# Performance work log

Measured on AMD Instinct MI355X. Metric: run time of the kernel, lower is better.

The kernel has to match this reference:

```python
import jax, jax.numpy as jnp
import numpy as np
import math

S, D = 8192, 128

def setup_inputs() -> dict:
    key = jax.random.key(0)
    kq, kk, kv = jax.random.split(key, 3)
    return {
        "q": jax.random.normal(kq, (S, D), dtype=jnp.float32),
        "k": jax.random.normal(kk, (S, D), dtype=jnp.float32),
        "v": jax.random.normal(kv, (S, D), dtype=jnp.float32),
    }

def reference(q, k, v):
    # scores: [S, S]; scale by sqrt(d) as in the torch module
    scale = 1.0 / math.sqrt(q.shape[1])
    scores = (q @ k.T) * scale
    attn = jax.nn.softmax(scores, axis=-1)
    return attn @ v
```

## Files before the change

### kernel.cpp

```cpp
#include <hip/hip_runtime.h>
#include <hip/hip_bf16.h>

#define SEQ 8192
#define HD 128
#define BM 256
#define BN 64
#define NQT (SEQ / BM)
#define THREADS 1024

typedef __bf16 bf16_t;
typedef __bf16 bf16x2 __attribute__((ext_vector_type(2)));
typedef __bf16 bf16x8 __attribute__((ext_vector_type(8)));
typedef float f32x4 __attribute__((ext_vector_type(4)));
typedef float f32x16 __attribute__((ext_vector_type(16)));
typedef unsigned int u32x4 __attribute__((ext_vector_type(4)));

#if __has_builtin(__builtin_amdgcn_exp2f)
__device__ inline float exp2_fast(float x) { return __builtin_amdgcn_exp2f(x); }
#else
__device__ inline float exp2_fast(float x) { return exp2f(x); }
#endif

__device__ inline void permswap32(unsigned int& a, unsigned int& b) {
#if __has_builtin(__builtin_amdgcn_permlane32_swap)
  auto r = __builtin_amdgcn_permlane32_swap(a, b, false, false);
  a = (unsigned int)r[0];
  b = (unsigned int)r[1];
#else
  asm volatile("v_permlane32_swap_b32 %0, %1" : "+v"(a), "+v"(b));
#endif
}

__device__ inline void load_lds16(const void* g, void* l) {
  __builtin_amdgcn_global_load_lds(
      (const __attribute__((address_space(1))) void*)g,
      (__attribute__((address_space(3))) void*)l, 16, 0, 0);
}

#define SYNC()                                                             \
  do {                                                                     \
    asm volatile("s_waitcnt vmcnt(0) lgkmcnt(0)\n\ts_barrier" ::: "memory"); \
    __builtin_amdgcn_sched_barrier(0);                                     \
  } while (0)

__global__ __launch_bounds__(256) void prep_kernel(const float* __restrict__ K,
                                                   const float* __restrict__ V,
                                                   bf16_t* __restrict__ Kb,
                                                   bf16_t* __restrict__ VT) {
  const int b = (int)blockIdx.x;
  const int tid = (int)threadIdx.x;
  if (b < 256) {
    __shared__ float tile[64][65];
    const int T = b & 127;
    const int d0 = (b >> 7) * 64;
    const int s0 = T * 64;
    const int r = tid >> 2;
    const int c0 = (tid & 3) * 16;
#pragma unroll
    for (int j4 = 0; j4 < 4; ++j4) {
      float4 x = *(const float4*)&V[(size_t)(s0 + r) * HD + d0 + c0 + j4 * 4];
      tile[r][c0 + j4 * 4 + 0] = x.x;
      tile[r][c0 + j4 * 4 + 1] = x.y;
      tile[r][c0 + j4 * 4 + 2] = x.z;
      tile[r][c0 + j4 * 4 + 3] = x.w;
    }
    __syncthreads();
    const int d_l = tid & 63;
    const int kc0 = (tid >> 6) * 2;
#pragma unroll
    for (int k2 = 0; k2 < 2; ++k2) {
      const int kc = kc0 + k2;
      bf16x8 wv;
#pragma unroll
      for (int j = 0; j < 8; ++j) wv[j] = (bf16_t)tile[kc * 8 + j][d_l];
      *(bf16x8*)&VT[((size_t)(T * 8 + kc) * 128 + d0 + d_l) * 8] = wv;
    }
  } else {
    const int base = (b - 256) * 2048 + tid * 8;
    const int row = base >> 7;
    const int c = (base >> 3) & 15;
    const int T = row >> 6;
    const int r = row & 63;
    float4 a = *(const float4*)&K[base];
    float4 cc = *(const float4*)&K[base + 4];
    bf16x8 f;
    f[0] = (bf16_t)a.x; f[1] = (bf16_t)a.y; f[2] = (bf16_t)a.z; f[3] = (bf16_t)a.w;
    f[4] = (bf16_t)cc.x; f[5] = (bf16_t)cc.y; f[6] = (bf16_t)cc.z; f[7] = (bf16_t)cc.w;
    *(bf16x8*)&Kb[((size_t)(T * 16 + c) * 64 + r) * 8] = f;
  }
}

__global__ __launch_bounds__(THREADS, 4) void fattn_kernel(
    const float* __restrict__ Q, const bf16_t* __restrict__ Kb,
    const bf16_t* __restrict__ VT, float* __restrict__ Opart,
    float* __restrict__ Lpart, int kshift, int nit) {
  __shared__ __align__(16) bf16_t kt2[2][16][64][8];
  __shared__ __align__(16) bf16_t vt2[2][8][128][8];
  __shared__ __align__(16) char pbuf[2][8][4][64][16];

  const int tid = (int)threadIdx.x;
  const int lane = tid & 63;
  const int w = tid >> 6;
  const int qw = w & 7;
  const int h = lane >> 5;
  const int n32 = lane & 31;

  const int qt = (int)blockIdx.x >> kshift;
  const int sp = (int)blockIdx.x & ((1 << kshift) - 1);
  const int qbase = qt * BM;
  const int tile0 = sp * nit;

  const float SC2 = 0.08838834764831845f * 1.4426950408889634f;

  char* const ktB = (char*)&kt2[0][0][0][0];
  char* const vtB = (char*)&vt2[0][0][0][0];
  char* const pbB = (char*)&pbuf[0][0][0][0][0];

#define DMA_K(TILE, BUF)                                                   \
  _Pragma("unroll")                                                        \
  for (int t = 0; t < 2; ++t) {                                            \
    const int rr = qw * 2 + t;                                             \
    load_lds16(Kb + ((size_t)((TILE) * 16 + rr) * 64 + lane) * 8,          \
               ktB + (BUF) * 16384 + rr * 1024);                           \
  }
#define DMA_V(TILE, BUF)                                                   \
  _Pragma("unroll")                                                        \
  for (int t = 0; t < 2; ++t) {                                            \
    const int rr = qw * 2 + t;                                             \
    load_lds16(VT + ((size_t)((TILE) * 8 + (rr >> 1)) * 128 + (rr & 1) * 64 + lane) * 8, \
               vtB + (BUF) * 16384 + rr * 1024);                           \
  }

#define EXPPACKW(SACC, KK2, CIDX, BUF)                                     \
  {                                                                        \
    float pf[8];                                                           \
    _Pragma("unroll")                                                      \
    for (int j = 0; j < 8; ++j) pf[j] = exp2_fast((SACC)[8 * (KK2) + j]);  \
    l_acc += ((pf[0] + pf[1]) + (pf[2] + pf[3])) +                         \
             ((pf[4] + pf[5]) + (pf[6] + pf[7]));                          \
    bf16x2 p0, p1, p2, p3;                                                 \
    p0[0] = (bf16_t)pf[0]; p0[1] = (bf16_t)pf[1];                          \
    p1[0] = (bf16_t)pf[2]; p1[1] = (bf16_t)pf[3];                          \
    p2[0] = (bf16_t)pf[4]; p2[1] = (bf16_t)pf[5];                          \
    p3[0] = (bf16_t)pf[6]; p3[1] = (bf16_t)pf[7];                          \
    unsigned int sA = __builtin_bit_cast(unsigned int, p0);                \
    unsigned int sB = __builtin_bit_cast(unsigned int, p1);                \
    unsigned int sC = __builtin_bit_cast(unsigned int, p2);                \
    unsigned int sD = __builtin_bit_cast(unsigned int, p3);                \
    permswap32(sA, sC);                                                    \
    permswap32(sB, sD);                                                    \
    u32x4 fv;                                                              \
    fv[0] = sA; fv[1] = sB; fv[2] = sC; fv[3] = sD;                        \
    *(u32x4*)(pbB + (BUF) * 32768 + qw * 4096 + (CIDX) * 1024 + lane * 16) = fv; \
  }

#define QKBODY(IT, CUR)                                                    \
  {                                                                        \
    const int it_ = (IT);                                                  \
    if (it_ + 1 < nit) { DMA_K(tile0 + it_ + 1, (CUR) ^ 1) }               \
    f32x16 sacc0, sacc1;                                                   \
    _Pragma("unroll")                                                      \
    for (int e = 0; e < 16; ++e) { sacc0[e] = 0.f; sacc1[e] = 0.f; }       \
    _Pragma("unroll")                                                      \
    for (int kk = 0; kk < 8; ++kk) {                                       \
      bf16x8 af0 = *(const bf16x8*)(ktB + (CUR) * 16384 + (2 * kk + h) * 1024 + n32 * 16); \
      sacc0 = __builtin_amdgcn_mfma_f32_32x32x16_bf16(af0, qf[kk], sacc0, 0, 0, 0); \
      bf16x8 af1 = *(const bf16x8*)(ktB + (CUR) * 16384 + (2 * kk + h) * 1024 + (32 + n32) * 16); \
      sacc1 = __builtin_amdgcn_mfma_f32_32x32x16_bf16(af1, qf[kk], sacc1, 0, 0, 0); \
    }                                                                      \
    EXPPACKW(sacc0, 0, 0, CUR)                                             \
    EXPPACKW(sacc0, 1, 1, CUR)                                             \
    EXPPACKW(sacc1, 0, 2, CUR)                                             \
    EXPPACKW(sacc1, 1, 3, CUR)                                             \
    SYNC();                                                                \
  }

#define PVCOMP(PBUF)                                                       \
  _Pragma("unroll")                                                        \
  for (int C = 0; C < 4; ++C) {                                            \
    bf16x8 pa = *(const bf16x8*)(pbB + (PBUF) * 32768 + qw * 4096 + C * 1024 + lane * 16); \
    _Pragma("unroll")                                                      \
    for (int ot = 0; ot < 4; ++ot) {                                       \
      bf16x8 vb = *(const bf16x8*)(vtB + (PBUF) * 16384 + (C * 2 + h) * 2048 + \
                                   (ot * 32 + n32) * 16);                  \
      o_acc[ot] = __builtin_amdgcn_mfma_f32_32x32x16_bf16(pa, vb, o_acc[ot], 0, 0, 0); \
    }                                                                      \
  }

#define PVBODY(IT, CUR)                                                    \
  {                                                                        \
    DMA_V(tile0 + (IT), CUR)                                               \
    PVCOMP((CUR) ^ 1)                                                      \
    SYNC();                                                                \
  }

  if (w < 8) {
    bf16x8 qf[8];
    {
      const float* qp = Q + (size_t)(qbase + qw * 32 + n32) * HD + h * 8;
#pragma unroll
      for (int kk = 0; kk < 8; ++kk) {
        float4 a = *(const float4*)(qp + kk * 16);
        float4 b = *(const float4*)(qp + kk * 16 + 4);
        bf16x8 f;
        f[0] = (bf16_t)(a.x * SC2); f[1] = (bf16_t)(a.y * SC2);
        f[2] = (bf16_t)(a.z * SC2); f[3] = (bf16_t)(a.w * SC2);
        f[4] = (bf16_t)(b.x * SC2); f[5] = (bf16_t)(b.y * SC2);
        f[6] = (bf16_t)(b.z * SC2); f[7] = (bf16_t)(b.w * SC2);
        qf[kk] = f;
      }
    }
    float l_acc = 0.f;

    DMA_K(tile0, 0)
    SYNC();

    for (int it = 0; it < nit; it += 2) {
      QKBODY(it, 0)
      QKBODY(it + 1, 1)
    }

    float l = l_acc + __shfl_xor(l_acc, 32);
    if (lane < 32)
      Lpart[(size_t)sp * SEQ + qbase + qw * 32 + n32] = l;
  } else {
    f32x16 o_acc[4];
#pragma unroll
    for (int i = 0; i < 4; ++i)
#pragma unroll
      for (int e = 0; e < 16; ++e) o_acc[i][e] = 0.f;

    SYNC();

    DMA_V(tile0, 0)
    SYNC();
    PVBODY(1, 1)
    for (int it = 2; it < nit; it += 2) {
      PVBODY(it, 0)
      PVBODY(it + 1, 1)
    }
    PVCOMP(1)

    float* op = Opart + ((size_t)sp * SEQ + qbase + qw * 32) * HD;
#pragma unroll
    for (int ot = 0; ot < 4; ++ot)
#pragma unroll
      for (int reg = 0; reg < 16; ++reg) {
        const int row = (reg & 3) + 8 * (reg >> 2) + 4 * h;
        op[row * HD + ot * 32 + n32] = o_acc[ot][reg];
      }
  }

#undef QKBODY
#undef PVBODY
#undef PVCOMP
#undef EXPPACKW
#undef DMA_K
#undef DMA_V
}

__global__ __launch_bounds__(256) void combine_kernel(const float* __restrict__ Opart,
                                                      const float* __restrict__ Lpart,
                                                      float* __restrict__ out, int ksplit) {
  const int tid = (int)threadIdx.x;
  const int row = (int)blockIdx.x * 8 + (tid >> 5);
  const int c0 = (tid & 31) * 4;
  float lsum = 0.f;
  for (int s = 0; s < ksplit; ++s) lsum += Lpart[(size_t)s * SEQ + row];
  f32x4 acc;
#pragma unroll
  for (int e = 0; e < 4; ++e) acc[e] = 0.f;
  for (int s = 0; s < ksplit; ++s) {
    f32x4 o = *(const f32x4*)&Opart[((size_t)s * SEQ + row) * HD + c0];
#pragma unroll
    for (int e = 0; e < 4; ++e) acc[e] += o[e];
  }
  const float inv = 1.0f / lsum;
  f32x4 res;
#pragma unroll
  for (int e = 0; e < 4; ++e) res[e] = acc[e] * inv;
  *(f32x4*)&out[(size_t)row * HD + c0] = res;
}

extern "C" void kernel_launch(void* const* d_in, const int* in_sizes, int n_in,
                              void* d_out, int out_size, void* d_ws, size_t ws_size,
                              hipStream_t stream) {
  const float* Q = (const float*)d_in[0];
  const float* K = (const float*)d_in[1];
  const float* V = (const float*)d_in[2];
  float* out = (float*)d_out;

  int ksplit = 8, kshift = 3;
  while (ksplit > 1) {
    size_t need = (size_t)ksplit * SEQ * HD * 4
                + (size_t)ksplit * SEQ * 4
                + (size_t)SEQ * HD * 2 * 2;
    if (need <= ws_size) break;
    ksplit >>= 1; kshift--;
  }

  char* ws = (char*)d_ws;
  float* Opart = (float*)ws;
  float* Lpart = (float*)(ws + (size_t)ksplit * SEQ * HD * 4);
  bf16_t* Kb = (bf16_t*)(ws + (size_t)ksplit * SEQ * HD * 4 + (size_t)ksplit * SEQ * 4);
  bf16_t* VT = Kb + (size_t)SEQ * HD;

  const int nit = SEQ / (ksplit * BN);

  prep_kernel<<<768, 256, 0, stream>>>(K, V, Kb, VT);
  fattn_kernel<<<NQT * ksplit, THREADS, 0, stream>>>(Q, Kb, VT, Opart, Lpart, kshift, nit);
  combine_kernel<<<SEQ / 8, 256, 0, stream>>>(Opart, Lpart, out, ksplit);
}
```

Before: 108.6 us.

## Rebalance warp specialization to 4 QK waves and 8 PV waves

Reduces the block from 16 to 12 waves. Each of 4 QK waves now handles two 32-row query groups, reusing each loaded K fragment for two MFMAs. Each of 8 PV waves computes a 2x2 block of 32x32 tiles (two query groups by half of head dim), reusing P and V fragments across MFMAs. The aim is fewer LDS reads per MFMA and a better balance between producer and consumer waves. In exchange, QK waves keep twice the Q fragments and accumulators, raising register pressure, and QK throughput per block is concentrated in fewer waves.

Result: slower. 126.3 us (+16.3%).

```diff
diff --git a/kernel.cpp b/kernel.cpp
--- a/kernel.cpp
+++ b/kernel.cpp
@@ -6,7 +6,7 @@
 #define BM 256
 #define BN 64
 #define NQT (SEQ / BM)
-#define THREADS 1024
+#define THREADS 768
 
 typedef __bf16 bf16_t;
 typedef __bf16 bf16x2 __attribute__((ext_vector_type(2)));
@@ -90,7 +90,7 @@
   }
 }
 
-__global__ __launch_bounds__(THREADS, 4) void fattn_kernel(
+__global__ __launch_bounds__(THREADS, 3) void fattn_kernel(
     const float* __restrict__ Q, const bf16_t* __restrict__ Kb,
     const bf16_t* __restrict__ VT, float* __restrict__ Opart,
     float* __restrict__ Lpart, int kshift, int nit) {
@@ -101,7 +101,6 @@
   const int tid = (int)threadIdx.x;
   const int lane = tid & 63;
   const int w = tid >> 6;
-  const int qw = w & 7;
   const int h = lane >> 5;
   const int n32 = lane & 31;
 
@@ -118,26 +117,26 @@
 
 #define DMA_K(TILE, BUF)                                                   \
   _Pragma("unroll")                                                        \
-  for (int t = 0; t < 2; ++t) {                                            \
-    const int rr = qw * 2 + t;                                             \
+  for (int t = 0; t < 4; ++t) {                                            \
+    const int rr = w * 4 + t;                                              \
     load_lds16(Kb + ((size_t)((TILE) * 16 + rr) * 64 + lane) * 8,          \
                ktB + (BUF) * 16384 + rr * 1024);                           \
   }
 #define DMA_V(TILE, BUF)                                                   \
   _Pragma("unroll")                                                        \
   for (int t = 0; t < 2; ++t) {                                            \
-    const int rr = qw * 2 + t;                                             \
+    const int rr = (w - 4) * 2 + t;                                        \
     load_lds16(VT + ((size_t)((TILE) * 8 + (rr >> 1)) * 128 + (rr & 1) * 64 + lane) * 8, \
                vtB + (BUF) * 16384 + rr * 1024);                           \
   }
 
-#define EXPPACKW(SACC, KK2, CIDX, BUF)                                     \
+#define EXPPACKW(SACC, KK2, QG, CIDX, BUF, LACC)                           \
   {                                                                        \
     float pf[8];                                                           \
     _Pragma("unroll")                                                      \
     for (int j = 0; j < 8; ++j) pf[j] = exp2_fast((SACC)[8 * (KK2) + j]);  \
-    l_acc += ((pf[0] + pf[1]) + (pf[2] + pf[3])) +                         \
-             ((pf[4] + pf[5]) + (pf[6] + pf[7]));                          \
+    LACC += ((pf[0] + pf[1]) + (pf[2] + pf[3])) +                          \
+            ((pf[4] + pf[5]) + (pf[6] + pf[7]));                           \
     bf16x2 p0, p1, p2, p3;                                                 \
     p0[0] = (bf16_t)pf[0]; p0[1] = (bf16_t)pf[1];                          \
     p1[0] = (bf16_t)pf[2]; p1[1] = (bf16_t)pf[3];                          \
@@ -151,40 +150,45 @@
     permswap32(sB, sD);                                                    \
     u32x4 fv;                                                              \
     fv[0] = sA; fv[1] = sB; fv[2] = sC; fv[3] = sD;                        \
-    *(u32x4*)(pbB + (BUF) * 32768 + qw * 4096 + (CIDX) * 1024 + lane * 16) = fv; \
+    *(u32x4*)(pbB + (BUF) * 32768 + (QG) * 4096 + (CIDX) * 1024 + lane * 16) = fv; \
   }
 
 #define QKBODY(IT, CUR)                                                    \
   {                                                                        \
     const int it_ = (IT);                                                  \
     if (it_ + 1 < nit) { DMA_K(tile0 + it_ + 1, (CUR) ^ 1) }               \
-    f32x16 sacc0, sacc1;                                                   \
+    f32x16 s00, s10, s01, s11;                     \
     _Pragma("unroll")                                                      \
-    for (int e = 0; e < 16; ++e) { sacc0[e] = 0.f; sacc1[e] = 0.f; }       \
+    for (int e = 0; e < 16; ++e) { s00[e] = 0.f; s10[e] = 0.f; s01[e] = 0.f; s11[e] = 0.f; } \
     _Pragma("unroll")                                                      \
     for (int kk = 0; kk < 8; ++kk) {                                       \
       bf16x8 af0 = *(const bf16x8*)(ktB + (CUR) * 16384 + (2 * kk + h) * 1024 + n32 * 16); \
-      sacc0 = __builtin_amdgcn_mfma_f32_32x32x16_bf16(af0, qf[kk], sacc0, 0, 0, 0); \
       bf16x8 af1 = *(const bf16x8*)(ktB + (CUR) * 16384 + (2 * kk + h) * 1024 + (32 + n32) * 16); \
-      sacc1 = __builtin_amdgcn_mfma_f32_32x32x16_bf16(af1, qf[kk], sacc1, 0, 0, 0); \
+      s00 = __builtin_amdgcn_mfma_f32_32x32x16_bf16(af0, qf[0][kk], s00, 0, 0, 0); \
+      s10 = __builtin_amdgcn_mfma_f32_32x32x16_bf16(af1, qf[0][kk], s10, 0, 0, 0); \
+      s01 = __builtin_amdgcn_mfma_f32_32x32x16_bf16(af0, qf[1][kk], s01, 0, 0, 0); \
+      s11 = __builtin_amdgcn_mfma_f32_32x32x16_bf16(af1, qf[1][kk], s11, 0, 0, 0); \
     }                                                                      \
-    EXPPACKW(sacc0, 0, 0, CUR)                                             \
-    EXPPACKW(sacc0, 1, 1, CUR)                                             \
-    EXPPACKW(sacc1, 0, 2, CUR)                                             \
-    EXPPACKW(sacc1, 1, 3, CUR)                                             \
+    EXPPACKW(s00, 0, g0, 0, CUR, l_acc0) EXPPACKW(s00, 1, g0, 1, CUR, l_acc0) \
+    EXPPACKW(s10, 0, g0, 2, CUR, l_acc0) EXPPACKW(s10, 1, g0, 3, CUR, l_acc0) \
+    EXPPACKW(s01, 0, g1, 0, CUR, l_acc1) EXPPACKW(s01, 1, g1, 1, CUR, l_acc1) \
+    EXPPACKW(s11, 0, g1, 2, CUR, l_acc1) EXPPACKW(s11, 1, g1, 3, CUR, l_acc1) \
     SYNC();                                                                \
   }
 
 #define PVCOMP(PBUF)                                                       \
   _Pragma("unroll")                                                        \
   for (int C = 0; C < 4; ++C) {                                            \
-    bf16x8 pa = *(const bf16x8*)(pbB + (PBUF) * 32768 + qw * 4096 + C * 1024 + lane * 16); \
-    _Pragma("unroll")                                                      \
-    for (int ot = 0; ot < 4; ++ot) {                                       \
-      bf16x8 vb = *(const bf16x8*)(vtB + (PBUF) * 16384 + (C * 2 + h) * 2048 + \
-                                   (ot * 32 + n32) * 16);                  \
-      o_acc[ot] = __builtin_amdgcn_mfma_f32_32x32x16_bf16(pa, vb, o_acc[ot], 0, 0, 0); \
-    }                                                                      \
+    bf16x8 pa0 = *(const bf16x8*)(pbB + (PBUF) * 32768 + g0 * 4096 + C * 1024 + lane * 16); \
+    bf16x8 pa1 = *(const bf16x8*)(pbB + (PBUF) * 32768 + g1 * 4096 + C * 1024 + lane * 16); \
+    bf16x8 vb0 = *(const bf16x8*)(vtB + (PBUF) * 16384 + (C * 2 + h) * 2048 + \
+                                  (dh * 64 + n32) * 16);                   \
+    bf16x8 vb1 = *(const bf16x8*)(vtB + (PBUF) * 16384 + (C * 2 + h) * 2048 + \
+                                  (dh * 64 + 32 + n32) * 16);              \
+    o_acc00 = __builtin_amdgcn_mfma_f32_32x32x16_bf16(pa0, vb0, o_acc00, 0, 0, 0); \
+    o_acc01 = __builtin_amdgcn_mfma_f32_32x32x16_bf16(pa0, vb1, o_acc01, 0, 0, 0); \
+    o_acc10 = __builtin_amdgcn_mfma_f32_32x32x16_bf16(pa1, vb0, o_acc10, 0, 0, 0); \
+    o_acc11 = __builtin_amdgcn_mfma_f32_32x32x16_bf16(pa1, vb1, o_acc11, 0, 0, 0); \
   }
 
 #define PVBODY(IT, CUR)                                                    \
@@ -194,10 +198,12 @@
     SYNC();                                                                \
   }
 
-  if (w < 8) {
-    bf16x8 qf[8];
-    {
-      const float* qp = Q + (size_t)(qbase + qw * 32 + n32) * HD + h * 8;
+  if (w < 4) {
+    const int g0 = 2 * w, g1 = 2 * w + 1;
+    bf16x8 qf[2][8];
+#pragma unroll
+    for (int j = 0; j < 2; ++j) {
+      const float* qp = Q + (size_t)(qbase + (2 * w + j) * 32 + n32) * HD + h * 8;
 #pragma unroll
       for (int kk = 0; kk < 8; ++kk) {
         float4 a = *(const float4*)(qp + kk * 16);
@@ -207,10 +213,10 @@
         f[2] = (bf16_t)(a.z * SC2); f[3] = (bf16_t)(a.w * SC2);
         f[4] = (bf16_t)(b.x * SC2); f[5] = (bf16_t)(b.y * SC2);
         f[6] = (bf16_t)(b.z * SC2); f[7] = (bf16_t)(b.w * SC2);
-        qf[kk] = f;
+        qf[j][kk] = f;
       }
     }
-    float l_acc = 0.f;
+    float l_acc0 = 0.f, l_acc1 = 0.f;
 
     DMA_K(tile0, 0)
     SYNC();
@@ -220,15 +226,21 @@
       QKBODY(it + 1, 1)
     }
 
-    float l = l_acc + __shfl_xor(l_acc, 32);
-    if (lane < 32)
-      Lpart[(size_t)sp * SEQ + qbase + qw * 32 + n32] = l;
+    float l0 = l_acc0 + __shfl_xor(l_acc0, 32);
+    float l1 = l_acc1 + __shfl_xor(l_acc1, 32);
+    if (lane < 32) {
+      Lpart[(size_t)sp * SEQ + qbase + g0 * 32 + n32] = l0;
+      Lpart[(size_t)sp * SEQ + qbase + g1 * 32 + n32] = l1;
+    }
   } else {
-    f32x16 o_acc[4];
-#pragma unroll
-    for (int i = 0; i < 4; ++i)
-#pragma unroll
-      for (int e = 0; e < 16; ++e) o_acc[i][e] = 0.f;
+    const int p = w - 4;
+    const int g0 = (p & 3) * 2, g1 = g0 + 1;
+    const int dh = p >> 2;
+    f32x16 o_acc00, o_acc01, o_acc10, o_acc11;
+#pragma unroll
+    for (int e = 0; e < 16; ++e) {
+      o_acc00[e] = 0.f; o_acc01[e] = 0.f; o_acc10[e] = 0.f; o_acc11[e] = 0.f;
+    }
 
     SYNC();
 
@@ -241,14 +253,18 @@
     }
     PVCOMP(1)
 
-    float* op = Opart + ((size_t)sp * SEQ + qbase + qw * 32) * HD;
-#pragma unroll
-    for (int ot = 0; ot < 4; ++ot)
+#pragma unroll
+    for (int g = 0; g < 2; ++g) {
+      float* op = Opart + ((size_t)sp * SEQ + qbase + (g0 + g) * 32) * HD + dh * 64;
+      const f32x16& oa0 = g ? o_acc10 : o_acc00;
+      const f32x16& oa1 = g ? o_acc11 : o_acc01;
 #pragma unroll
       for (int reg = 0; reg < 16; ++reg) {
         const int row = (reg & 3) + 8 * (reg >> 2) + 4 * h;
-        op[row * HD + ot * 32 + n32] = o_acc[ot][reg];
+        op[row * HD + n32] = oa0[reg];
+        op[row * HD + 32 + n32] = oa1[reg];
       }
+    }
   }
 
 #undef QKBODY
```
